# Optimization experiments

Hardware: AMD Instinct MI355X
Metric: run time of the kernel (lower is better)

Reference implementation:

```python
import jax, jax.numpy as jnp
import numpy as np

K = 512
RATE = 0.999

def _l2norm(v):
    # matches torch F.normalize(dim=1): v / max(||v||, 1e-12)
    n = jnp.linalg.norm(v, axis=1, keepdims=True)
    return v / jnp.maximum(n, 1e-12)

def setup_inputs() -> dict:
    key = jax.random.key(0)
    k1, k2 = jax.random.split(key)
    x = jax.random.normal(k1, (16, 256, 64, 64), dtype=jnp.float32)
    m = jax.random.normal(k2, (K, 256), dtype=jnp.float32)
    return {"x": x, "m": m}

def reference(x, m):
    b, c, h, w = x.shape
    xf = x.transpose(0, 2, 3, 1).reshape(-1, c)          # (n, c)
    xn = _l2norm(xf)
    mn = _l2norm(m)
    score = xn @ mn.T                                     # (n, k)
    # EMA codebook update (uses detached x in the original)
    xd = jax.lax.stop_gradient(xf)
    embed_ind = jnp.argmax(score, axis=1)                 # (n,)
    embed_sum = jax.ops.segment_sum(xd, embed_ind, num_segments=K)   # (k, c)
    counts = jax.ops.segment_sum(jnp.ones(xd.shape[0], xd.dtype), embed_ind, num_segments=K)
    embed_mean = embed_sum / (counts[:, None] + 1e-6)
    new_m = m * RATE + embed_mean * (1.0 - RATE)          # (k, c)
    # re-score against updated codebook
    mn2 = _l2norm(new_m)
    score2 = xn @ mn2.T                                   # (n, k)
    soft_label = jax.nn.softmax(score2, axis=1)
    out = soft_label @ new_m                              # (n, c)
    out = out.reshape(b, h, w, c).transpose(0, 3, 1, 2)   # (b, c, h, w)
    return out, score2
```

## Files before the change

kernel.cpp:

```cpp
#include <hip/hip_runtime.h>

#define Bb 16
#define Cc 256
#define HW 4096
#define Nn 65536
#define Kk 512

typedef __attribute__((ext_vector_type(4))) float f32x4;
typedef __attribute__((ext_vector_type(8))) short short8;

__device__ __forceinline__ float bf2f(unsigned int u){
  union { float f; unsigned int i; } v; v.i = u << 16; return v.f;
}
__device__ __forceinline__ unsigned short f2bf(float f){
  unsigned int i = __float_as_uint(f);
  unsigned int r = (i + 0x7fffu + ((i >> 16) & 1u)) >> 16;
  return (unsigned short)r;
}

__device__ __forceinline__ void gld_lds16(const char* g, char* lbase){
#if __has_builtin(__builtin_amdgcn_global_load_lds)
  __builtin_amdgcn_global_load_lds(
      (const __attribute__((address_space(1))) unsigned int*)g,
      (__attribute__((address_space(3))) unsigned int*)lbase, 16, 0, 0);
#else
  *reinterpret_cast<int4*>(lbase + (threadIdx.x & 63) * 16) =
      *reinterpret_cast<const int4*>(g);
#endif
}


__global__ __launch_bounds__(64) void k_mnorm(const float* __restrict__ m,
                                              unsigned short* __restrict__ mnf){
  int k = blockIdx.x, l = threadIdx.x;
  float4 v = *reinterpret_cast<const float4*>(m + (size_t)k * Cc + l * 4);
  float ss = v.x*v.x + v.y*v.y + v.z*v.z + v.w*v.w;
  #pragma unroll
  for (int off = 1; off < 64; off <<= 1) ss += __shfl_xor(ss, off, 64);
  float rn = 1.0f / fmaxf(sqrtf(ss), 1e-12f);
  ushort4 o;
  o.x = f2bf(v.x*rn); o.y = f2bf(v.y*rn); o.z = f2bf(v.z*rn); o.w = f2bf(v.w*rn);
  int kw = k >> 6, kt = (k >> 4) & 3, li = k & 15;
  int c0 = l * 4;
  int ks = c0 >> 5, gr = (c0 >> 3) & 3, eo = (l & 1) * 4;
  size_t off8 = ((((size_t)(kw*4 + kt)*8 + ks)*16 + li)*4 + gr)*8 + eo;
  *reinterpret_cast<ushort4*>(mnf + off8) = o;
}

__global__ __launch_bounds__(512, 4) void k_prep_score(const float* __restrict__ x,
                                                       const unsigned short* __restrict__ mnf,
                                                       float* __restrict__ rs,
                                                       unsigned short* __restrict__ xr,
                                                       int* __restrict__ eind){
  __shared__ __align__(16) char ldsB[32768];
  __shared__ float red[8][64];
  __shared__ float smax[8][64];
  __shared__ int   sidx[8][64];
  int t = threadIdx.x, w = t >> 6, l = t & 63, gr = l >> 4, li = l & 15;
  int b = blockIdx.x >> 6;
  int hw0 = (blockIdx.x & 63) << 6;
  const float* src = x + ((size_t)b * Cc + w * 32) * HW + hw0 + l;
  float ss = 0.f;
  unsigned int pk[16];
  #pragma unroll
  for (int j = 0; j < 16; ++j){
    float v0 = src[(size_t)(2*j    ) * HW];
    float v1 = src[(size_t)(2*j + 1) * HW];
    ss += v0 * v0 + v1 * v1;
    pk[j] = (unsigned int)f2bf(v0) | ((unsigned int)f2bf(v1) << 16);
  }
  #pragma unroll
  for (int q = 0; q < 4; ++q){
    int colb = w * 64 + q * 16;
    int4 vv;
    vv.x = (int)pk[q*4+0]; vv.y = (int)pk[q*4+1];
    vv.z = (int)pk[q*4+2]; vv.w = (int)pk[q*4+3];
    *reinterpret_cast<int4*>(ldsB + l * 512 + (colb ^ ((l & 7) << 4))) = vv;
  }
  red[w][l] = ss;
  int loff = li * 32 + gr * 8;
  short8 bv0[4];
  #pragma unroll
  for (int nt = 0; nt < 4; ++nt)
    bv0[nt] = *reinterpret_cast<const short8*>(
        mnf + ((size_t)(w*4 + nt)*8 + 0)*512 + loff);
  __syncthreads();
  if (t < 64){
    float s = 0.f;
    #pragma unroll
    for (int ww = 0; ww < 8; ++ww) s += red[ww][t];
    rs[(size_t)b * HW + hw0 + t] = 1.0f / fmaxf(sqrtf(s), 1e-12f);
  }
  f32x4 acc[4][4];
  #pragma unroll
  for (int mt = 0; mt < 4; ++mt)
    #pragma unroll
    for (int nt = 0; nt < 4; ++nt)
      acc[mt][nt] = (f32x4){0.f,0.f,0.f,0.f};
  #pragma unroll
  for (int ks = 0; ks < 8; ++ks){
    short8 af[4];
    #pragma unroll
    for (int mt = 0; mt < 4; ++mt){
      int row = mt * 16 + li;
      af[mt] = *reinterpret_cast<const short8*>(
          ldsB + row * 512 + ((ks * 64 + gr * 16) ^ ((row & 7) << 4)));
    }
    #pragma unroll
    for (int nt = 0; nt < 4; ++nt){
      short8 bv = (ks == 0) ? bv0[nt]
          : *reinterpret_cast<const short8*>(
                mnf + ((size_t)(w*4 + nt)*8 + ks)*512 + loff);
      #pragma unroll
      for (int mt = 0; mt < 4; ++mt)
        acc[mt][nt] = __builtin_amdgcn_mfma_f32_16x16x32_bf16(af[mt], bv, acc[mt][nt], 0, 0, 0);
    }
  }
  #pragma unroll
  for (int mt = 0; mt < 4; ++mt){
    #pragma unroll
    for (int r = 0; r < 4; ++r){
      float best = acc[mt][0][r]; int bi = w * 64 + li;
      #pragma unroll
      for (int nt = 1; nt < 4; ++nt){
        float v = acc[mt][nt][r]; int ii = w * 64 + nt * 16 + li;
        if (v > best){ best = v; bi = ii; }
      }
      #pragma unroll
      for (int off = 1; off < 16; off <<= 1){
        float ov = __shfl_xor(best, off, 64);
        int   oi = __shfl_xor(bi,   off, 64);
        if (ov > best || (ov == best && oi < bi)){ best = ov; bi = oi; }
      }
      if (li == 0){ int pr = mt * 16 + gr * 4 + r; smax[w][pr] = best; sidx[w][pr] = bi; }
    }
  }
  __syncthreads();
  if (t < 64){
    float best = smax[0][t]; int bi = sidx[0][t];
    #pragma unroll
    for (int ww = 1; ww < 8; ++ww){
      float v = smax[ww][t]; int ii = sidx[ww][t];
      if (v > best || (v == best && ii < bi)){ best = v; bi = ii; }
    }
    eind[(size_t)b * HW + hw0 + t] = bi;
  }
  char* dst = reinterpret_cast<char*>(xr) + ((size_t)b * HW + hw0) * 512;
  #pragma unroll
  for (int i = 0; i < 4; ++i){
    int px = i * 16 + (t >> 5);
    int colb = (t & 31) * 16;
    int4 rv = *reinterpret_cast<const int4*>(ldsB + px * 512 + (colb ^ ((px & 7) << 4)));
    *reinterpret_cast<int4*>(dst + (size_t)px * 512 + colb) = rv;
  }
}

__global__ __launch_bounds__(256) void k_segsum(const int* __restrict__ eind,
                                                const unsigned short* __restrict__ xr,
                                                float* __restrict__ es4,
                                                float* __restrict__ ec4){
  int kk = blockIdx.x >> 2, qr = blockIdx.x & 3;
  int t = threadIdx.x, w = t >> 6, l = t & 63;
  float a0=0.f,a1=0.f,a2=0.f,a3=0.f;
  int cnt = 0;
  int base = qr * 16384 + w * 4096;
  for (int it = 0; it < 16; ++it){
    int pxb = base + it * 256;
    int4 e = *reinterpret_cast<const int4*>(eind + pxb + l * 4);
    #pragma unroll
    for (int comp = 0; comp < 4; ++comp){
      int ev = comp == 0 ? e.x : comp == 1 ? e.y : comp == 2 ? e.z : e.w;
      unsigned long long mask = __ballot(ev == kk);
      cnt += (int)__popcll(mask);
      while (mask){
        int src = __ffsll((unsigned long long)mask) - 1;
        mask &= mask - 1;
        int px = pxb + src * 4 + comp;
        ushort4 uv = *reinterpret_cast<const ushort4*>(xr + (size_t)px * Cc + l * 4);
        a0 += bf2f(uv.x); a1 += bf2f(uv.y);
        a2 += bf2f(uv.z); a3 += bf2f(uv.w);
      }
    }
  }
  __shared__ float red[4][256];
  __shared__ float rcnt[4];
  red[w][l*4+0]=a0; red[w][l*4+1]=a1; red[w][l*4+2]=a2; red[w][l*4+3]=a3;
  if (l == 0) rcnt[w] = (float)cnt;
  __syncthreads();
  float s = red[0][t] + red[1][t] + red[2][t] + red[3][t];
  es4[(size_t)blockIdx.x * Cc + t] = s;
  if (t == 0) ec4[blockIdx.x] = rcnt[0] + rcnt[1] + rcnt[2] + rcnt[3];
}

__global__ __launch_bounds__(64) void k_update(const float* __restrict__ es4,
                                               const float* __restrict__ ec4,
                                               const float* __restrict__ m,
                                               unsigned short* __restrict__ mn2f,
                                               unsigned short* __restrict__ nmTf){
  int k = blockIdx.x, l = threadIdx.x;
  float sx = 0.f, sy = 0.f, sz = 0.f, sw = 0.f, cs = 0.f;
  #pragma unroll
  for (int q = 0; q < 4; ++q){
    float4 s = *reinterpret_cast<const float4*>(es4 + ((size_t)(4*k+q)) * Cc + l * 4);
    sx += s.x; sy += s.y; sz += s.z; sw += s.w;
    cs += ec4[4*k+q];
  }
  float4 mv = *reinterpret_cast<const float4*>(m + (size_t)k * Cc + l * 4);
  float inv = 1.0f / (cs + 1e-6f);
  float nx = mv.x * 0.999f + sx * inv * 0.001f;
  float ny = mv.y * 0.999f + sy * inv * 0.001f;
  float nz = mv.z * 0.999f + sz * inv * 0.001f;
  float nw = mv.w * 0.999f + sw * inv * 0.001f;
  float ss = nx*nx + ny*ny + nz*nz + nw*nw;
  #pragma unroll
  for (int off = 1; off < 64; off <<= 1) ss += __shfl_xor(ss, off, 64);
  float rn = 1.0f / fmaxf(sqrtf(ss), 1e-12f);
  ushort4 o;
  o.x = f2bf(nx*rn); o.y = f2bf(ny*rn); o.z = f2bf(nz*rn); o.w = f2bf(nw*rn);
  {
    int kw = k >> 6, kt = (k >> 4) & 3, li = k & 15;
    int c0 = l * 4;
    int ks = c0 >> 5, gr = (c0 >> 3) & 3, eo = (l & 1) * 4;
    size_t off8 = ((((size_t)(kw*4 + kt)*8 + ks)*16 + li)*4 + gr)*8 + eo;
    *reinterpret_cast<ushort4*>(mn2f + off8) = o;
  }
  {
    int ksn = k >> 5, grn = (k >> 3) & 3, en = k & 7;
    unsigned short nv[4] = {f2bf(nx), f2bf(ny), f2bf(nz), f2bf(nw)};
    #pragma unroll
    for (int q = 0; q < 4; ++q){
      int c = l * 4 + q;
      int cb = c >> 4, li2 = c & 15;
      size_t off8 = ((((size_t)cb*16 + ksn)*16 + li2)*4 + grn)*8 + en;
      nmTf[off8] = nv[q];
    }
  }
}

__global__ __launch_bounds__(512, 2) void k_out(const unsigned short* __restrict__ xr,
                                                const float* __restrict__ rs,
                                                const unsigned short* __restrict__ mn2f,
                                                const unsigned short* __restrict__ nmTf,
                                                float* __restrict__ out,
                                                float* __restrict__ score2){
  __shared__ __align__(16) char smem[131072];
  __shared__ float wbuf[8 * 128];
  __shared__ float rz[128];
  __shared__ float rsl[128];
  int t = threadIdx.x, w = t >> 6, l = t & 63, gr = l >> 4, li = l & 15;
  int px0 = blockIdx.x * 128;
  const char* gsrc = reinterpret_cast<const char*>(xr + (size_t)px0 * Cc);
  #pragma unroll
  for (int j = 0; j < 8; ++j){
    int chunk = j * 512 + t;
    int rr = chunk >> 5, slot = chunk & 31;
    const char* g = gsrc + rr * 512 + ((slot * 16) ^ ((rr & 7) << 4));
    int rr0 = (j * 512 + w * 64) >> 5;
    gld_lds16(g, smem + rr0 * 512);
  }
  int loff = li * 32 + gr * 8;
  short8 amc[4];
  #pragma unroll
  for (int kt = 0; kt < 4; ++kt)
    amc[kt] = *reinterpret_cast<const short8*>(
        mn2f + ((size_t)(w*4 + kt)*8 + 0)*512 + loff);
  if (t < 128) rsl[t] = rs[px0 + t];
  __syncthreads();
  f32x4 acc[4][8];
  #pragma unroll
  for (int kt = 0; kt < 4; ++kt)
    #pragma unroll
    for (int pt = 0; pt < 8; ++pt)
      acc[kt][pt] = (f32x4){0.f,0.f,0.f,0.f};
  int kw = w * 64;
  #pragma unroll
  for (int ks = 0; ks < 8; ++ks){
    short8 amn[4];
    if (ks < 7){
      #pragma unroll
      for (int kt = 0; kt < 4; ++kt)
        amn[kt] = *reinterpret_cast<const short8*>(
            mn2f + ((size_t)(w*4 + kt)*8 + (ks+1))*512 + loff);
    }
    #pragma unroll
    for (int pt = 0; pt < 8; ++pt){
      int row = pt * 16 + li;
      short8 bx = *reinterpret_cast<const short8*>(
          smem + row * 512 + ((ks * 64 + gr * 16) ^ ((row & 7) << 4)));
      #pragma unroll
      for (int kt = 0; kt < 4; ++kt)
        acc[kt][pt] = __builtin_amdgcn_mfma_f32_16x16x32_bf16(amc[kt], bx, acc[kt][pt], 0, 0, 0);
    }
    if (ks < 7){
      #pragma unroll
      for (int kt = 0; kt < 4; ++kt) amc[kt] = amn[kt];
    }
  }
  __syncthreads();
  float s[8] = {0.f,0.f,0.f,0.f,0.f,0.f,0.f,0.f};
  #pragma unroll
  for (int kt = 0; kt < 4; ++kt){
    #pragma unroll
    for (int pt = 0; pt < 8; ++pt){
      int px = pt * 16 + li;
      float rsv = rsl[px];
      f32x4 v = acc[kt][pt];
      v[0] *= rsv; v[1] *= rsv; v[2] *= rsv; v[3] *= rsv;
      acc[kt][pt] = v;
      float p0 = __expf(v[0]), p1 = __expf(v[1]), p2 = __expf(v[2]), p3 = __expf(v[3]);
      s[pt] += (p0 + p1) + (p2 + p3);
      unsigned int lo = (unsigned int)f2bf(p0) | ((unsigned int)f2bf(p1) << 16);
      unsigned int hi = (unsigned int)f2bf(p2) | ((unsigned int)f2bf(p3) << 16);
      int colb = (kw + kt * 16 + gr * 4) * 2;
      uint2 pv; pv.x = lo; pv.y = hi;
      *reinterpret_cast<uint2*>(smem + px * 1024 + (colb ^ ((px & 7) << 4))) = pv;
    }
  }
  #pragma unroll
  for (int pt = 0; pt < 8; ++pt){
    s[pt] += __shfl_xor(s[pt], 16, 64);
    s[pt] += __shfl_xor(s[pt], 32, 64);
  }
  if (gr == 0){
    #pragma unroll
    for (int pt = 0; pt < 8; ++pt) wbuf[w * 128 + pt * 16 + li] = s[pt];
  }
  short8 bvc[2];
  #pragma unroll
  for (int nt = 0; nt < 2; ++nt)
    bvc[nt] = *reinterpret_cast<const short8*>(
        nmTf + ((size_t)(w*2 + nt)*16 + 0)*512 + loff);
  __syncthreads();
  if (t < 128){
    float sum = 0.f;
    #pragma unroll
    for (int ww = 0; ww < 8; ++ww) sum += wbuf[ww * 128 + t];
    rz[t] = 1.0f / sum;
  }
  f32x4 acc2[8][2];
  #pragma unroll
  for (int mt = 0; mt < 8; ++mt)
    #pragma unroll
    for (int nt = 0; nt < 2; ++nt)
      acc2[mt][nt] = (f32x4){0.f,0.f,0.f,0.f};
  #pragma unroll
  for (int ks = 0; ks < 16; ++ks){
    short8 bvn[2];
    if (ks < 15){
      #pragma unroll
      for (int nt = 0; nt < 2; ++nt)
        bvn[nt] = *reinterpret_cast<const short8*>(
            nmTf + ((size_t)(w*2 + nt)*16 + (ks+1))*512 + loff);
    }
    #pragma unroll
    for (int mt = 0; mt < 8; ++mt){
      int row = mt * 16 + li;
      short8 af = *reinterpret_cast<const short8*>(
          smem + row * 1024 + ((ks * 64 + gr * 16) ^ ((row & 7) << 4)));
      #pragma unroll
      for (int nt = 0; nt < 2; ++nt)
        acc2[mt][nt] = __builtin_amdgcn_mfma_f32_16x16x32_bf16(af, bvc[nt], acc2[mt][nt], 0, 0, 0);
    }
    if (ks < 15){
      #pragma unroll
      for (int nt = 0; nt < 2; ++nt) bvc[nt] = bvn[nt];
    }
  }
  __syncthreads();
  float* s2 = score2 + (size_t)px0 * Kk;
  #pragma unroll
  for (int h = 0; h < 2; ++h){
    #pragma unroll
    for (int kt = 0; kt < 4; ++kt)
      #pragma unroll
      for (int pt2 = 0; pt2 < 4; ++pt2){
        int pxl = pt2 * 16 + li;
        int kb = (kw + kt * 16 + gr * 4) * 4;
        *reinterpret_cast<f32x4*>(smem + pxl * 2048 + (kb ^ ((pxl & 7) << 4)))
            = acc[kt][h * 4 + pt2];
      }
    __syncthreads();
    #pragma unroll
    for (int r = 0; r < 8; ++r){
      int pxl = w * 8 + r;
      int px = h * 64 + pxl;
      #pragma unroll
      for (int j = 0; j < 2; ++j){
        int o = j * 1024 + l * 16;
        f32x4 v = *reinterpret_cast<const f32x4*>(smem + pxl * 2048 + (o ^ ((pxl & 7) << 4)));
        *reinterpret_cast<f32x4*>(s2 + (size_t)px * Kk + (o >> 2)) = v;
      }
    }
    __syncthreads();
  }
  #pragma unroll
  for (int mt = 0; mt < 8; ++mt){
    int pb = mt * 16 + gr * 4;
    f32x4 rzv = *reinterpret_cast<const f32x4*>(&rz[pb]);
    #pragma unroll
    for (int nt = 0; nt < 2; ++nt){
      int c = w * 32 + nt * 16 + li;
      f32x4 v;
      v[0] = acc2[mt][nt][0] * rzv[0];
      v[1] = acc2[mt][nt][1] * rzv[1];
      v[2] = acc2[mt][nt][2] * rzv[2];
      v[3] = acc2[mt][nt][3] * rzv[3];
      *reinterpret_cast<f32x4*>(smem + c * 512 + ((pb * 4) ^ ((c & 7) << 4))) = v;
    }
  }
  __syncthreads();
  int b = px0 >> 12, hw0 = px0 & 4095;
  #pragma unroll
  for (int i = 0; i < 16; ++i){
    int c = w * 32 + i * 2 + (l >> 5);
    int o = (l & 31) * 16;
    f32x4 v = *reinterpret_cast<const f32x4*>(smem + c * 512 + (o ^ ((c & 7) << 4)));
    *reinterpret_cast<f32x4*>(out + ((size_t)b * Cc + c) * HW + hw0 + (o >> 2)) = v;
  }
}

extern "C" void kernel_launch(void* const* d_in, const int* in_sizes, int n_in,
                              void* d_out, int out_size, void* d_ws, size_t ws_size,
                              hipStream_t stream) {
  (void)in_sizes; (void)n_in; (void)out_size; (void)ws_size;
  const float* x = (const float*)d_in[0];
  const float* m = (const float*)d_in[1];
  float* out    = (float*)d_out;
  float* score2 = (float*)d_out + (size_t)Nn * Cc;

  char* ws = (char*)d_ws;
  unsigned short* xr   = (unsigned short*)(ws);
  float*          rsb  = (float*)(ws + 33554432);
  unsigned short* mnf  = (unsigned short*)(ws + 33816576);
  int*            ei   = (int*)(ws + 34078720);
  float*          es4  = (float*)(ws + 34340864);
  float*          ec4  = (float*)(ws + 36438016);
  unsigned short* mn2f = (unsigned short*)(ws + 36446208);
  unsigned short* nmTf = (unsigned short*)(ws + 36708352);

  k_mnorm       <<<512,  64,  0, stream>>>(m, mnf);
  k_prep_score  <<<1024, 512, 0, stream>>>(x, mnf, rsb, xr, ei);
  k_segsum      <<<2048, 256, 0, stream>>>(ei, xr, es4, ec4);
  k_update      <<<512,  64,  0, stream>>>(es4, ec4, m, mn2f, nmTf);
  k_out         <<<512,  512, 0, stream>>>(xr, rsb, mn2f, nmTf, out, score2);
}
```

Baseline: 149.7 us.

## Double pixel tile in prep_score and use nontemporal stores for outputs

The prep/score kernel now handles 128 pixels per block instead of 64. Each thread loads float2 pairs, the codebook fragments loaded from global are reused across twice as many MFMA rows, and the LDS swizzle is adjusted for the paired rows. Separately, the large score2 and output writes in k_out become nontemporal stores so they pollute the cache less. The costs are doubled LDS use, higher register pressure, half as many blocks (occupancy lowered to 2 per CU), and a smaller grid.

Result: slower. 155.9 us (+4.1%).

```diff
diff --git a/kernel.cpp b/kernel.cpp
--- a/kernel.cpp
+++ b/kernel.cpp
@@ -29,6 +29,10 @@
 #endif
 }
 
+__device__ __forceinline__ void nt_store4(float* p, f32x4 v){
+  __builtin_nontemporal_store(v, reinterpret_cast<f32x4*>(p));
+}
+
 
 __global__ __launch_bounds__(64) void k_mnorm(const float* __restrict__ m,
                                               unsigned short* __restrict__ mnf){
@@ -47,37 +51,45 @@
   *reinterpret_cast<ushort4*>(mnf + off8) = o;
 }
 
-__global__ __launch_bounds__(512, 4) void k_prep_score(const float* __restrict__ x,
+__global__ __launch_bounds__(512, 2) void k_prep_score(const float* __restrict__ x,
                                                        const unsigned short* __restrict__ mnf,
                                                        float* __restrict__ rs,
                                                        unsigned short* __restrict__ xr,
                                                        int* __restrict__ eind){
-  __shared__ __align__(16) char ldsB[32768];
-  __shared__ float red[8][64];
-  __shared__ float smax[8][64];
-  __shared__ int   sidx[8][64];
+  __shared__ __align__(16) char ldsB[65536];
+  __shared__ float red[8][128];
+  __shared__ float smax[8][128];
+  __shared__ int   sidx[8][128];
   int t = threadIdx.x, w = t >> 6, l = t & 63, gr = l >> 4, li = l & 15;
-  int b = blockIdx.x >> 6;
-  int hw0 = (blockIdx.x & 63) << 6;
-  const float* src = x + ((size_t)b * Cc + w * 32) * HW + hw0 + l;
-  float ss = 0.f;
-  unsigned int pk[16];
-  #pragma unroll
-  for (int j = 0; j < 16; ++j){
-    float v0 = src[(size_t)(2*j    ) * HW];
-    float v1 = src[(size_t)(2*j + 1) * HW];
-    ss += v0 * v0 + v1 * v1;
-    pk[j] = (unsigned int)f2bf(v0) | ((unsigned int)f2bf(v1) << 16);
-  }
-  #pragma unroll
-  for (int q = 0; q < 4; ++q){
-    int colb = w * 64 + q * 16;
-    int4 vv;
-    vv.x = (int)pk[q*4+0]; vv.y = (int)pk[q*4+1];
-    vv.z = (int)pk[q*4+2]; vv.w = (int)pk[q*4+3];
-    *reinterpret_cast<int4*>(ldsB + l * 512 + (colb ^ ((l & 7) << 4))) = vv;
-  }
-  red[w][l] = ss;
+  int b = blockIdx.x >> 5;
+  int hw0 = (blockIdx.x & 31) << 7;
+  const float* src = x + ((size_t)b * Cc + w * 32) * HW + hw0 + 2 * l;
+  float ss0 = 0.f, ss1 = 0.f;
+  unsigned int pk0[16], pk1[16];
+  #pragma unroll
+  for (int cj = 0; cj < 16; ++cj){
+    float2 a  = *reinterpret_cast<const float2*>(src + (size_t)(2*cj    ) * HW);
+    float2 c2 = *reinterpret_cast<const float2*>(src + (size_t)(2*cj + 1) * HW);
+    ss0 += a.x*a.x + c2.x*c2.x;
+    ss1 += a.y*a.y + c2.y*c2.y;
+    pk0[cj] = (unsigned int)f2bf(a.x) | ((unsigned int)f2bf(c2.x) << 16);
+    pk1[cj] = (unsigned int)f2bf(a.y) | ((unsigned int)f2bf(c2.y) << 16);
+  }
+  {
+    int p0 = 2 * l, p1 = 2 * l + 1;
+    int sw = ((p0 >> 1) & 7) << 4;
+    #pragma unroll
+    for (int q = 0; q < 4; ++q){
+      int colb = w * 64 + q * 16;
+      int4 v0; v0.x = (int)pk0[q*4]; v0.y = (int)pk0[q*4+1];
+      v0.z = (int)pk0[q*4+2]; v0.w = (int)pk0[q*4+3];
+      *reinterpret_cast<int4*>(ldsB + p0 * 512 + (colb ^ sw)) = v0;
+      int4 v1; v1.x = (int)pk1[q*4]; v1.y = (int)pk1[q*4+1];
+      v1.z = (int)pk1[q*4+2]; v1.w = (int)pk1[q*4+3];
+      *reinterpret_cast<int4*>(ldsB + p1 * 512 + (colb ^ sw)) = v1;
+    }
+    red[w][p0] = ss0; red[w][p1] = ss1;
+  }
   int loff = li * 32 + gr * 8;
   short8 bv0[4];
   #pragma unroll
@@ -85,26 +97,26 @@
     bv0[nt] = *reinterpret_cast<const short8*>(
         mnf + ((size_t)(w*4 + nt)*8 + 0)*512 + loff);
   __syncthreads();
-  if (t < 64){
+  if (t < 128){
     float s = 0.f;
     #pragma unroll
     for (int ww = 0; ww < 8; ++ww) s += red[ww][t];
     rs[(size_t)b * HW + hw0 + t] = 1.0f / fmaxf(sqrtf(s), 1e-12f);
   }
-  f32x4 acc[4][4];
-  #pragma unroll
-  for (int mt = 0; mt < 4; ++mt)
+  f32x4 acc[8][4];
+  #pragma unroll
+  for (int mt = 0; mt < 8; ++mt)
     #pragma unroll
     for (int nt = 0; nt < 4; ++nt)
       acc[mt][nt] = (f32x4){0.f,0.f,0.f,0.f};
   #pragma unroll
   for (int ks = 0; ks < 8; ++ks){
-    short8 af[4];
-    #pragma unroll
-    for (int mt = 0; mt < 4; ++mt){
+    short8 af[8];
+    #pragma unroll
+    for (int mt = 0; mt < 8; ++mt){
       int row = mt * 16 + li;
       af[mt] = *reinterpret_cast<const short8*>(
-          ldsB + row * 512 + ((ks * 64 + gr * 16) ^ ((row & 7) << 4)));
+          ldsB + row * 512 + ((ks * 64 + gr * 16) ^ (((row >> 1) & 7) << 4)));
     }
     #pragma unroll
     for (int nt = 0; nt < 4; ++nt){
@@ -112,12 +124,12 @@
           : *reinterpret_cast<const short8*>(
                 mnf + ((size_t)(w*4 + nt)*8 + ks)*512 + loff);
       #pragma unroll
-      for (int mt = 0; mt < 4; ++mt)
+      for (int mt = 0; mt < 8; ++mt)
         acc[mt][nt] = __builtin_amdgcn_mfma_f32_16x16x32_bf16(af[mt], bv, acc[mt][nt], 0, 0, 0);
     }
   }
   #pragma unroll
-  for (int mt = 0; mt < 4; ++mt){
+  for (int mt = 0; mt < 8; ++mt){
     #pragma unroll
     for (int r = 0; r < 4; ++r){
       float best = acc[mt][0][r]; int bi = w * 64 + li;
@@ -136,7 +148,7 @@
     }
   }
   __syncthreads();
-  if (t < 64){
+  if (t < 128){
     float best = smax[0][t]; int bi = sidx[0][t];
     #pragma unroll
     for (int ww = 1; ww < 8; ++ww){
@@ -147,10 +159,11 @@
   }
   char* dst = reinterpret_cast<char*>(xr) + ((size_t)b * HW + hw0) * 512;
   #pragma unroll
-  for (int i = 0; i < 4; ++i){
+  for (int i = 0; i < 8; ++i){
     int px = i * 16 + (t >> 5);
     int colb = (t & 31) * 16;
-    int4 rv = *reinterpret_cast<const int4*>(ldsB + px * 512 + (colb ^ ((px & 7) << 4)));
+    int4 rv = *reinterpret_cast<const int4*>(
+        ldsB + px * 512 + (colb ^ (((px >> 1) & 7) << 4)));
     *reinterpret_cast<int4*>(dst + (size_t)px * 512 + colb) = rv;
   }
 }
@@ -388,7 +401,7 @@
       for (int j = 0; j < 2; ++j){
         int o = j * 1024 + l * 16;
         f32x4 v = *reinterpret_cast<const f32x4*>(smem + pxl * 2048 + (o ^ ((pxl & 7) << 4)));
-        *reinterpret_cast<f32x4*>(s2 + (size_t)px * Kk + (o >> 2)) = v;
+        nt_store4(s2 + (size_t)px * Kk + (o >> 2), v);
       }
     }
     __syncthreads();
@@ -415,7 +428,7 @@
     int c = w * 32 + i * 2 + (l >> 5);
     int o = (l & 31) * 16;
     f32x4 v = *reinterpret_cast<const f32x4*>(smem + c * 512 + (o ^ ((c & 7) << 4)));
-    *reinterpret_cast<f32x4*>(out + ((size_t)b * Cc + c) * HW + hw0 + (o >> 2)) = v;
+    nt_store4(out + ((size_t)b * Cc + c) * HW + hw0 + (o >> 2), v);
   }
 }
 
@@ -439,7 +452,7 @@
   unsigned short* nmTf = (unsigned short*)(ws + 36708352);
 
   k_mnorm       <<<512,  64,  0, stream>>>(m, mnf);
-  k_prep_score  <<<1024, 512, 0, stream>>>(x, mnf, rsb, xr, ei);
+  k_prep_score  <<<512,  512, 0, stream>>>(x, mnf, rsb, xr, ei);
   k_segsum      <<<2048, 256, 0, stream>>>(ei, xr, es4, ec4);
   k_update      <<<512,  64,  0, stream>>>(es4, ec4, m, mn2f, nmTf);
   k_out         <<<512,  512, 0, stream>>>(xr, rsb, mn2f, nmTf, out, score2);
```
